# Optimization experiments

Hardware: AMD Instinct MI355X
Metric: run time of the kernel (lower is better)

The kernel has to match this reference:

```python
import jax, jax.numpy as jnp
import numpy as np

B, S, E, H, K = 64, 512, 256, 512, 100


def setup_inputs() -> dict:
    key = jax.random.key(0)
    ks = jax.random.split(key, 7)
    scale = 0.02
    return {
        "event_types": jax.random.randint(ks[0], (B, S), 0, K),
        "time_deltas": jax.random.uniform(ks[1], (B, S), dtype=jnp.float32),
        "embedding": jax.random.normal(ks[2], (K, E), dtype=jnp.float32) * scale,
        "W": jax.random.normal(ks[3], (E + H, 5 * H), dtype=jnp.float32) * scale,
        "b": jnp.zeros((5 * H,), dtype=jnp.float32),
        "Wi": jax.random.normal(ks[4], (H, K), dtype=jnp.float32) * scale,
        "bi": jnp.zeros((K,), dtype=jnp.float32),
    }


def _ctlstm_scan(x_seq, dt_seq, W, b, hidden_dim):
    """x_seq: [B,S,E], dt_seq: [B,S]. Returns h_seq [B,S,H], decay_seq [B,S,H]."""
    bsz = x_seq.shape[0]
    h0 = jnp.zeros((bsz, hidden_dim), x_seq.dtype)
    c0 = jnp.zeros((bsz, hidden_dim), x_seq.dtype)

    def step(carry, inp):
        h, c = carry
        x_t, dt_t = inp  # [B,E], [B]
        z = jnp.concatenate([x_t, h], axis=-1) @ W + b  # [B,5H]
        i, f, o, g, d = jnp.split(z, 5, axis=-1)
        i = jax.nn.sigmoid(i)
        f = jax.nn.sigmoid(f)
        o = jax.nn.sigmoid(o)
        g = jnp.tanh(g)
        decay = jax.nn.softplus(d)  # decay rate >= 0
        c_new = f * c + i * g
        c_t = c_new * jnp.exp(-decay * dt_t[:, None])  # continuous-time decay
        h_t = o * jnp.tanh(c_t)
        return (h_t, c_t), (h_t, decay)

    # time-major for scan
    xs = (jnp.swapaxes(x_seq, 0, 1), jnp.swapaxes(dt_seq, 0, 1))
    _, (h_seq, decay_seq) = jax.lax.scan(step, (h0, c0), xs)
    return jnp.swapaxes(h_seq, 0, 1), jnp.swapaxes(decay_seq, 0, 1)


def reference(event_types, time_deltas, embedding, W, b, Wi, bi):
    x_seq = embedding[event_types]  # [B,S,E]
    hidden_state, decay_rate = _ctlstm_scan(x_seq, time_deltas, W, b, H)
    base_intensities = jax.nn.softplus(hidden_state @ Wi + bi)  # [B,S,K]
    return hidden_state, decay_rate, base_intensities
```

## Files before the change

### kernel.cpp

```cpp
#include <hip/hip_runtime.h>
#include <hip/hip_bf16.h>
#include <stdint.h>

#define BB 64
#define SS 512
#define EE 256
#define HH 512
#define K5 2560
#define NWG 32

typedef short s16x8 __attribute__((ext_vector_type(8)));
typedef float vf4 __attribute__((ext_vector_type(4)));

#define OFF_WBT   0UL
#define OFF_EMB   3932160UL
#define OFF_WIT   3983360UL
#define OFF_DTT   4098048UL
#define OFF_FLAGS 4229120UL
#define OFF_HBUF  4294656UL
#define OFF_ZXP   37849088UL

__device__ __forceinline__ unsigned short f2bf(float f) {
  unsigned u = __float_as_uint(f);
  u += 0x7fffu + ((u >> 16) & 1u);
  return (unsigned short)(u >> 16);
}
__device__ __forceinline__ float bf2f(unsigned short h) {
  return __uint_as_float(((unsigned)h) << 16);
}
__device__ __forceinline__ float sigmoidf_(float x) { return 1.f / (1.f + __expf(-x)); }
__device__ __forceinline__ float softplusf_(float x) {
  return fmaxf(x, 0.f) + log1pf(__expf(-fabsf(x)));
}
__device__ __forceinline__ float tanhf_(float x) {
  float e = __expf(2.f * x);
  return 1.f - 2.f / (e + 1.f);
}

__global__ void init_kernel(const float* __restrict__ W, const float* __restrict__ emb,
                            const float* __restrict__ Wi, const float* __restrict__ td,
                            unsigned short* __restrict__ WbT, unsigned short* __restrict__ embB,
                            unsigned short* __restrict__ WiT, float* __restrict__ dtT,
                            int* __restrict__ flags) {
  unsigned i = blockIdx.x * 256u + threadIdx.x;
  if (i < 1966080u) {
    unsigned c = i / 768u, k = i % 768u;
    WbT[i] = f2bf(W[(size_t)k * 2560u + c]);
    return;
  }
  i -= 1966080u;
  if (i < 25600u) { embB[i] = f2bf(emb[i]); return; }
  i -= 25600u;
  if (i < 57344u) {
    unsigned c = i / 512u, k = i % 512u;
    WiT[i] = f2bf(c < 100u ? Wi[(size_t)k * 100u + c] : 0.f);
    return;
  }
  i -= 57344u;
  if (i < 32768u) {
    unsigned t = i / 64u, b = i % 64u;
    dtT[i] = td[(size_t)b * 512u + t];
    return;
  }
  i -= 32768u;
  if (i < 16384u) { flags[i] = 0; return; }
}

__global__ __launch_bounds__(256, 2)
void zx_kernel(const int* __restrict__ evt, const unsigned short* __restrict__ embB,
               const unsigned short* __restrict__ WbT, const float* __restrict__ bias,
               unsigned short* __restrict__ zxp) {
  const int t = blockIdx.y;
  const int tid = threadIdx.x;
  const int v = tid >> 6, lane = tid & 63;
  const int m = lane & 15, quad = lane >> 4;
  const int cbase = blockIdx.x * 256 + v * 64;

  s16x8 Breg[8][4];
#pragma unroll
  for (int cf = 0; cf < 4; ++cf) {
    const unsigned short* bp = WbT + (size_t)(cbase + cf * 16 + m) * 768 + quad * 8;
#pragma unroll
    for (int ch = 0; ch < 8; ++ch) Breg[ch][cf] = *(const s16x8*)(bp + ch * 32);
  }
  int ev[4];
#pragma unroll
  for (int rt = 0; rt < 4; ++rt) ev[rt] = evt[(size_t)(rt * 16 + m) * 512 + t];

  vf4 acc[4][4];
#pragma unroll
  for (int cf = 0; cf < 4; ++cf) {
    float bbv = bias[cbase + cf * 16 + m];
#pragma unroll
    for (int rt = 0; rt < 4; ++rt) acc[rt][cf] = (vf4){bbv, bbv, bbv, bbv};
  }
#pragma unroll
  for (int ch = 0; ch < 8; ++ch) {
#pragma unroll
    for (int rt = 0; rt < 4; ++rt) {
      s16x8 a = *(const s16x8*)(embB + (size_t)ev[rt] * 256 + ch * 32 + quad * 8);
#pragma unroll
      for (int cf = 0; cf < 4; ++cf)
        acc[rt][cf] = __builtin_amdgcn_mfma_f32_16x16x32_bf16(a, Breg[ch][cf], acc[rt][cf], 0, 0, 0);
    }
  }
#pragma unroll
  for (int cf = 0; cf < 4; ++cf) {
    int col0 = cbase + cf * 16;
    int g = col0 >> 9;
    int w = (col0 & 511) >> 4;
#pragma unroll
    for (int rt = 0; rt < 4; ++rt) {
      unsigned h0 = f2bf(acc[rt][cf][0]);
      unsigned h1 = f2bf(acc[rt][cf][1]);
      unsigned h2 = f2bf(acc[rt][cf][2]);
      unsigned h3 = f2bf(acc[rt][cf][3]);
      uint2 val;
      val.x = h0 | (h1 << 16);
      val.y = h2 | (h3 << 16);
      ((uint2*)zxp)[((((size_t)t * 32 + w) * 4 + rt) * 5 + g) * 64 + lane] = val;
    }
  }
}

__global__ __launch_bounds__(256, 1)
void scan_kernel(const unsigned short* __restrict__ WbT,
                 const unsigned short* __restrict__ zxp,
                 const float* __restrict__ dtT,
                 unsigned short* __restrict__ hbuf,
                 int* __restrict__ flags,
                 float* __restrict__ out_h, float* __restrict__ out_d) {
  const int w = blockIdx.x;
  const int tid = threadIdx.x;
  const int v = tid >> 6, lane = tid & 63;
  const int m = lane & 15, quad = lane >> 4;
  const int rowb = v * 16;
  const int bb0 = rowb + quad * 4;
  const int col = w * 16 + m;

  s16x8 Breg[16][5];
#pragma unroll
  for (int g = 0; g < 5; ++g) {
    const unsigned short* bp = WbT + (size_t)(g * 512 + w * 16 + m) * 768 + 256 + quad * 8;
#pragma unroll
    for (int ch = 0; ch < 16; ++ch) Breg[ch][g] = *(const s16x8*)(bp + ch * 32);
  }

  vf4 cst = (vf4){0.f, 0.f, 0.f, 0.f};

  for (int t = 0; t < 512; ++t) {
    vf4 acc[5];
#pragma unroll
    for (int g = 0; g < 5; ++g) {
      uint2 zv = ((const uint2*)zxp)[((((size_t)t * 32 + w) * 4 + v) * 5 + g) * 64 + lane];
      acc[g][0] = bf2f((unsigned short)(zv.x & 0xffffu));
      acc[g][1] = bf2f((unsigned short)(zv.x >> 16));
      acc[g][2] = bf2f((unsigned short)(zv.y & 0xffffu));
      acc[g][3] = bf2f((unsigned short)(zv.y >> 16));
    }
    vf4 dt4 = *(const vf4*)(dtT + t * 64 + bb0);

    if (t > 0) {
      const int* fp = flags + (t - 1) * NWG + (lane & 31);
      while (__hip_atomic_load(fp, __ATOMIC_RELAXED, __HIP_MEMORY_SCOPE_AGENT) == 0) {
        __builtin_amdgcn_s_sleep(1);
      }
      __builtin_amdgcn_fence(__ATOMIC_ACQUIRE, "agent");
      const unsigned short* hsrc =
          hbuf + (size_t)(t - 1) * (BB * HH) + (size_t)(rowb + m) * HH + quad * 8;
#pragma unroll
      for (int ch = 0; ch < 16; ++ch) {
        s16x8 a = *(const s16x8*)(hsrc + ch * 32);
#pragma unroll
        for (int g = 0; g < 5; ++g)
          acc[g] = __builtin_amdgcn_mfma_f32_16x16x32_bf16(a, Breg[ch][g], acc[g], 0, 0, 0);
      }
    }

#pragma unroll
    for (int r = 0; r < 4; ++r) {
      float i_ = sigmoidf_(acc[0][r]);
      float f_ = sigmoidf_(acc[1][r]);
      float o_ = sigmoidf_(acc[2][r]);
      float g_ = tanhf_(acc[3][r]);
      float dec = softplusf_(acc[4][r]);
      float cn = f_ * cst[r] + i_ * g_;
      float ct = cn * __expf(-dec * dt4[r]);
      float h_ = o_ * tanhf_(ct);
      cst[r] = ct;
      int b_ = bb0 + r;
      size_t oo = ((size_t)b_ * SS + t) * HH + col;
      out_h[oo] = h_;
      out_d[oo] = dec;
      __hip_atomic_store(hbuf + (size_t)t * (BB * HH) + (size_t)b_ * HH + col, f2bf(h_),
                         __ATOMIC_RELAXED, __HIP_MEMORY_SCOPE_AGENT);
    }
    __syncthreads();
    if (tid == 0)
      __hip_atomic_store(flags + t * NWG + w, 1, __ATOMIC_RELEASE, __HIP_MEMORY_SCOPE_AGENT);
  }
}

__global__ __launch_bounds__(256, 2)
void inten_kernel(const unsigned short* __restrict__ hbuf,
                  const unsigned short* __restrict__ WiT,
                  const float* __restrict__ bi,
                  float* __restrict__ out_i) {
  const int b = blockIdx.y;
  const int t0 = blockIdx.x * 64;
  const int tid = threadIdx.x;
  const int v = tid >> 6, lane = tid & 63;
  const int m = lane & 15, quad = lane >> 4;
  const int trow = t0 + v * 16 + m;

  vf4 acc[7];
#pragma unroll
  for (int cf = 0; cf < 7; ++cf) {
    int c = cf * 16 + m;
    float bbv = (c < 100) ? bi[c] : 0.f;
    acc[cf] = (vf4){bbv, bbv, bbv, bbv};
  }
  const unsigned short* ha = hbuf + ((size_t)trow * 64 + b) * 512 + quad * 8;
#pragma unroll 4
  for (int ch = 0; ch < 16; ++ch) {
    s16x8 a = *(const s16x8*)(ha + ch * 32);
#pragma unroll
    for (int cf = 0; cf < 7; ++cf) {
      s16x8 bf = *(const s16x8*)(WiT + (size_t)(cf * 16 + m) * 512 + ch * 32 + quad * 8);
      acc[cf] = __builtin_amdgcn_mfma_f32_16x16x32_bf16(a, bf, acc[cf], 0, 0, 0);
    }
  }
#pragma unroll
  for (int cf = 0; cf < 7; ++cf) {
    int c = cf * 16 + m;
#pragma unroll
    for (int r = 0; r < 4; ++r) {
      int tt = t0 + v * 16 + quad * 4 + r;
      if (c < 100) out_i[((size_t)b * 512 + tt) * 100 + c] = softplusf_(acc[cf][r]);
    }
  }
}

extern "C" void kernel_launch(void* const* d_in, const int* in_sizes, int n_in,
                              void* d_out, int out_size, void* d_ws, size_t ws_size,
                              hipStream_t stream) {
  (void)in_sizes; (void)n_in; (void)out_size; (void)ws_size;
  const int*   evt  = (const int*)d_in[0];
  const float* td   = (const float*)d_in[1];
  const float* emb  = (const float*)d_in[2];
  const float* W    = (const float*)d_in[3];
  const float* bias = (const float*)d_in[4];
  const float* Wi   = (const float*)d_in[5];
  const float* bi   = (const float*)d_in[6];

  char* ws = (char*)d_ws;
  unsigned short* WbT  = (unsigned short*)(ws + OFF_WBT);
  unsigned short* embB = (unsigned short*)(ws + OFF_EMB);
  unsigned short* WiT  = (unsigned short*)(ws + OFF_WIT);
  float*          dtT  = (float*)(ws + OFF_DTT);
  int*            flags= (int*)(ws + OFF_FLAGS);
  unsigned short* hbuf = (unsigned short*)(ws + OFF_HBUF);
  unsigned short* zxp  = (unsigned short*)(ws + OFF_ZXP);

  float* out_h = (float*)d_out;
  float* out_d = out_h + (size_t)BB * SS * HH;
  float* out_i = out_d + (size_t)BB * SS * HH;

  init_kernel<<<8196, 256, 0, stream>>>(W, emb, Wi, td, WbT, embB, WiT, dtT, flags);
  zx_kernel<<<dim3(10, 512), 256, 0, stream>>>(evt, embB, WbT, bias, zxp);
  scan_kernel<<<NWG, 256, 0, stream>>>(WbT, zxp, dtT, hbuf, flags, out_h, out_d);
  inten_kernel<<<dim3(8, 64), 256, 0, stream>>>(hbuf, WiT, bi, out_i);
}
```

Baseline: 4.464 ms.

## Use per-wavefront flags to drop block barrier in LSTM scan handshake

Each wavefront now publishes its own ready flag after draining its own stores with s_waitcnt, so the per-step __syncthreads and the single-thread release store go away. Consumers poll 32x4 flags laid out in 16-step packed groups and use only a compiler barrier instead of an acquire fence. The fp32 output stores move after the flag publish so they stay off the critical handshake path. The risk is memory ordering: relaxed atomics plus waitcnt without a cache-level release/acquire fence may not guarantee visibility at agent scope.

Result: faster. 3.703 ms (-17.1%).

```diff
diff --git a/kernel.cpp b/kernel.cpp
--- a/kernel.cpp
+++ b/kernel.cpp
@@ -6,7 +6,6 @@
 #define SS 512
 #define EE 256
 #define HH 512
-#define K5 2560
 #define NWG 32
 
 typedef short s16x8 __attribute__((ext_vector_type(8)));
@@ -17,8 +16,12 @@
 #define OFF_WIT   3983360UL
 #define OFF_DTT   4098048UL
 #define OFF_FLAGS 4229120UL
-#define OFF_HBUF  4294656UL
-#define OFF_ZXP   37849088UL
+#define OFF_HBUF  4491264UL
+#define OFF_ZXP   38045696UL
+
+__device__ __forceinline__ int fidx(int t, int w, int v) {
+  return (((t >> 4) * 128) + w * 4 + v) * 16 + (t & 15);
+}
 
 __device__ __forceinline__ unsigned short f2bf(float f) {
   unsigned u = __float_as_uint(f);
@@ -63,7 +66,7 @@
     return;
   }
   i -= 32768u;
-  if (i < 16384u) { flags[i] = 0; return; }
+  if (i < 65536u) { flags[i] = 0; return; }
 }
 
 __global__ __launch_bounds__(256, 2)
@@ -161,13 +164,16 @@
     vf4 dt4 = *(const vf4*)(dtT + t * 64 + bb0);
 
     if (t > 0) {
-      const int* fp = flags + (t - 1) * NWG + (lane & 31);
-      while (__hip_atomic_load(fp, __ATOMIC_RELAXED, __HIP_MEMORY_SCOPE_AGENT) == 0) {
-        __builtin_amdgcn_s_sleep(1);
+      const int tp = t - 1;
+      if (lane < 32) {
+        const int* fp = flags + fidx(tp, lane, v);
+        while (__hip_atomic_load(fp, __ATOMIC_RELAXED, __HIP_MEMORY_SCOPE_AGENT) == 0) {
+          __builtin_amdgcn_s_sleep(1);
+        }
       }
-      __builtin_amdgcn_fence(__ATOMIC_ACQUIRE, "agent");
+      __asm__ __volatile__("" ::: "memory");
       const unsigned short* hsrc =
-          hbuf + (size_t)(t - 1) * (BB * HH) + (size_t)(rowb + m) * HH + quad * 8;
+          hbuf + (size_t)tp * (BB * HH) + (size_t)(rowb + m) * HH + quad * 8;
 #pragma unroll
       for (int ch = 0; ch < 16; ++ch) {
         s16x8 a = *(const s16x8*)(hsrc + ch * 32);
@@ -177,6 +183,7 @@
       }
     }
 
+    float hv[4], dv[4];
 #pragma unroll
     for (int r = 0; r < 4; ++r) {
       float i_ = sigmoidf_(acc[0][r]);
@@ -188,16 +195,23 @@
       float ct = cn * __expf(-dec * dt4[r]);
       float h_ = o_ * tanhf_(ct);
       cst[r] = ct;
-      int b_ = bb0 + r;
-      size_t oo = ((size_t)b_ * SS + t) * HH + col;
-      out_h[oo] = h_;
-      out_d[oo] = dec;
-      __hip_atomic_store(hbuf + (size_t)t * (BB * HH) + (size_t)b_ * HH + col, f2bf(h_),
-                         __ATOMIC_RELAXED, __HIP_MEMORY_SCOPE_AGENT);
-    }
-    __syncthreads();
-    if (tid == 0)
-      __hip_atomic_store(flags + t * NWG + w, 1, __ATOMIC_RELEASE, __HIP_MEMORY_SCOPE_AGENT);
+      hv[r] = h_; dv[r] = dec;
+      __hip_atomic_store(hbuf + (size_t)t * (BB * HH) + (size_t)(bb0 + r) * HH + col,
+                         f2bf(h_), __ATOMIC_RELAXED, __HIP_MEMORY_SCOPE_AGENT);
+    }
+    __asm__ __volatile__("" ::: "memory");
+    __builtin_amdgcn_s_waitcnt(0);
+    __asm__ __volatile__("" ::: "memory");
+    if (lane == 0) {
+      __hip_atomic_store(flags + fidx(t, w, v), 1, __ATOMIC_RELAXED,
+                         __HIP_MEMORY_SCOPE_AGENT);
+    }
+#pragma unroll
+    for (int r = 0; r < 4; ++r) {
+      size_t oo = ((size_t)(bb0 + r) * SS + t) * HH + col;
+      out_h[oo] = hv[r];
+      out_d[oo] = dv[r];
+    }
   }
 }
 
@@ -266,7 +280,7 @@
   float* out_d = out_h + (size_t)BB * SS * HH;
   float* out_i = out_d + (size_t)BB * SS * HH;
 
-  init_kernel<<<8196, 256, 0, stream>>>(W, emb, Wi, td, WbT, embB, WiT, dtT, flags);
+  init_kernel<<<8390, 256, 0, stream>>>(W, emb, Wi, td, WbT, embB, WiT, dtT, flags);
   zx_kernel<<<dim3(10, 512), 256, 0, stream>>>(evt, embB, WbT, bias, zxp);
   scan_kernel<<<NWG, 256, 0, stream>>>(WbT, zxp, dtT, hbuf, flags, out_h, out_d);
   inten_kernel<<<dim3(8, 64), 256, 0, stream>>>(hbuf, WiT, bi, out_i);
```
